# Optimization experiments

Hardware: AMD Instinct MI355X
Metric: run time of the kernel (lower is better)

## Reference

```python
import jax, jax.numpy as jnp
import numpy as np

B, C_MAX, T = 128, 272, 512
D1 = 320
NUM_SUBJECTS = 8
NUM_CHANNELS = [272, 256, 240, 224, 208, 270, 260, 248]


def setup_inputs() -> dict:
    key = jax.random.key(0)
    k_x, k_w, k_s = jax.random.split(key, 3)
    X = jax.random.normal(k_x, (B, C_MAX, T), dtype=jnp.float32)
    subject_idxs = jax.random.randint(k_s, (B,), 0, NUM_SUBJECTS)
    # Per-subject Conv1d(kernel=1, bias=False) weights, padded to C_MAX.
    # Original module only reads the first num_channels[s] input channels;
    # zeroing the padded columns reproduces that exactly.
    W = jax.random.normal(k_w, (NUM_SUBJECTS, D1, C_MAX), dtype=jnp.float32) * 0.02
    mask = np.zeros((NUM_SUBJECTS, 1, C_MAX), dtype=np.float32)
    for s, nc in enumerate(NUM_CHANNELS):
        mask[s, 0, :nc] = 1.0
    W = W * jnp.asarray(mask)
    return {"X": X, "subject_idxs": subject_idxs, "W": W}


def reference(X, subject_idxs, W):
    # Gather per-sample weight matrix [B, D1, C_MAX] by subject id, then
    # batched 1x1 conv == matmul over channels at every time step.
    Wsel = W[subject_idxs]                      # [B, D1, C]
    out = jnp.einsum("bdc,bct->bdt", Wsel, X)   # [B, D1, T]
    return out
```

## Files before the change

kernel.cpp:

```cpp
#include <hip/hip_runtime.h>

#define BB    128
#define CC    272
#define TT    512
#define DD1   320
#define KC    32
#define NCHUNK 9
#define NT    64
#define MT    160
#define LDA   40
#define LDB   40

typedef float  f32x4  __attribute__((ext_vector_type(4)));
typedef __bf16 bf16x4 __attribute__((ext_vector_type(4)));
typedef __bf16 bf16x8 __attribute__((ext_vector_type(8)));

#define BAR() asm volatile("s_waitcnt lgkmcnt(0)\ns_barrier" ::: "memory")

__global__ __launch_bounds__(256, 4)
void subj_conv_mfma(const float* __restrict__ X,
                    const int*   __restrict__ sidx,
                    const float* __restrict__ W,
                    float*       __restrict__ out) {
    const int b  = blockIdx.x;
    const int T0 = blockIdx.y * NT;
    const int d0 = blockIdx.z * MT;
    const int s  = sidx[b];

    __shared__ __bf16 As[MT * LDA];
    __shared__ __bf16 Bs[NT * LDB];

    const int tid  = threadIdx.x;
    const int lane = tid & 63;
    const int wv   = tid >> 6;
    const int wm   = wv & 1;
    const int wn   = wv >> 1;
    const int quad = lane >> 4;
    const int l16  = lane & 15;

    const float* Wb = W + ((size_t)s * DD1 + d0) * CC;
    const float* Xb = X + (size_t)b * CC * TT + T0;

    const int am  = tid >> 3;
    const int akk = (tid & 7) * 4;
    const int bcr = tid >> 4;
    const int bt  = (tid & 15) * 4;

    f32x4 acc[5][2];
#pragma unroll
    for (int mt = 0; mt < 5; ++mt) {
        acc[mt][0] = (f32x4){0.f, 0.f, 0.f, 0.f};
        acc[mt][1] = (f32x4){0.f, 0.f, 0.f, 0.f};
    }

    float4 pa[5];
    float4 pb[2];

    {
        const int c0 = 0;
#pragma unroll
        for (int p = 0; p < 5; ++p) {
            const int m = am + 32 * p;
            pa[p] = *(const float4*)(Wb + (size_t)m * CC + (c0 + akk));
        }
#pragma unroll
        for (int p = 0; p < 2; ++p) {
            const int c = c0 + bcr + 16 * p;
            pb[p] = *(const float4*)(Xb + (size_t)c * TT + bt);
        }
    }

    for (int kc = 0; kc < NCHUNK; ++kc) {
#pragma unroll
        for (int p = 0; p < 5; ++p) {
            const int m = am + 32 * p;
            bf16x4 h = {(__bf16)pa[p].x, (__bf16)pa[p].y,
                        (__bf16)pa[p].z, (__bf16)pa[p].w};
            *(bf16x4*)&As[m * LDA + akk] = h;
        }
#pragma unroll
        for (int p = 0; p < 2; ++p) {
            const int cr = bcr + 16 * p;
            Bs[(bt + 0) * LDB + cr] = (__bf16)pb[p].x;
            Bs[(bt + 1) * LDB + cr] = (__bf16)pb[p].y;
            Bs[(bt + 2) * LDB + cr] = (__bf16)pb[p].z;
            Bs[(bt + 3) * LDB + cr] = (__bf16)pb[p].w;
        }

        BAR();

        if (kc + 1 < NCHUNK) {
            const int c0 = (kc + 1) * KC;
#pragma unroll
            for (int p = 0; p < 5; ++p) {
                const int m = am + 32 * p;
                const int c = c0 + akk;
                float4 v = make_float4(0.f, 0.f, 0.f, 0.f);
                if (c < CC) v = *(const float4*)(Wb + (size_t)m * CC + c);
                pa[p] = v;
            }
#pragma unroll
            for (int p = 0; p < 2; ++p) {
                const int c = c0 + bcr + 16 * p;
                float4 v = make_float4(0.f, 0.f, 0.f, 0.f);
                if (c < CC) v = *(const float4*)(Xb + (size_t)c * TT + bt);
                pb[p] = v;
            }
        }

        bf16x8 bfr[2];
#pragma unroll
        for (int nt = 0; nt < 2; ++nt)
            bfr[nt] = *(const bf16x8*)&Bs[(wn * 32 + nt * 16 + l16) * LDB + quad * 8];

#pragma unroll
        for (int mt = 0; mt < 5; ++mt) {
            bf16x8 af = *(const bf16x8*)&As[(wm * 80 + mt * 16 + l16) * LDA + quad * 8];
#pragma unroll
            for (int nt = 0; nt < 2; ++nt)
                acc[mt][nt] = __builtin_amdgcn_mfma_f32_16x16x32_bf16(
                    af, bfr[nt], acc[mt][nt], 0, 0, 0);
        }

        BAR();
    }

#pragma unroll
    for (int mt = 0; mt < 5; ++mt) {
        const int d = d0 + wm * 80 + mt * 16 + quad * 4;
#pragma unroll
        for (int nt = 0; nt < 2; ++nt) {
            float* ob = out + ((size_t)b * DD1 + d) * TT + T0 + wn * 32 + nt * 16 + l16;
#pragma unroll
            for (int r = 0; r < 4; ++r)
                ob[(size_t)r * TT] = acc[mt][nt][r];
        }
    }
}

extern "C" void kernel_launch(void* const* d_in, const int* in_sizes, int n_in,
                              void* d_out, int out_size, void* d_ws, size_t ws_size,
                              hipStream_t stream) {
    const float* X    = (const float*)d_in[0];
    const int*   sidx = (const int*)  d_in[1];
    const float* W    = (const float*)d_in[2];
    float*       out  = (float*)d_out;

    dim3 grid(BB, TT / NT, 2);
    dim3 block(256);
    subj_conv_mfma<<<grid, block, 0, stream>>>(X, sidx, W, out);
}
```

Measured before the change: 168.2 us.

## Double-buffer LDS tiles and store X as fp32 row-major, converting on read

Adds two LDS buffers for both the W and X tiles so the next chunk is stored while the current one is consumed, cutting one barrier per iteration and looking two chunks ahead for global loads. The X tile is now kept in fp32 with its natural channel-major layout (padded stride 66) using vectorized float2 stores, instead of scattered transposed bf16 scalar stores. In exchange, each B fragment now takes eight scalar LDS reads plus conversions instead of one vector load, and LDS usage grows, which may reduce occupancy.

```diff
diff --git a/kernel.cpp b/kernel.cpp
--- a/kernel.cpp
+++ b/kernel.cpp
@@ -9,7 +9,7 @@
 #define NT    64
 #define MT    160
 #define LDA   40
-#define LDB   40
+#define LDB2  66
 
 typedef float  f32x4  __attribute__((ext_vector_type(4)));
 typedef __bf16 bf16x4 __attribute__((ext_vector_type(4)));
@@ -27,8 +27,8 @@
     const int d0 = blockIdx.z * MT;
     const int s  = sidx[b];
 
-    __shared__ __bf16 As[MT * LDA];
-    __shared__ __bf16 Bs[NT * LDB];
+    __shared__ __bf16 As[2][MT * LDA];
+    __shared__ float  Bs[2][KC * LDB2];
 
     const int tid  = threadIdx.x;
     const int lane = tid & 63;
@@ -56,73 +56,74 @@
     float4 pa[5];
     float4 pb[2];
 
-    {
-        const int c0 = 0;
+    auto load_chunk = [&](int c0) {
 #pragma unroll
         for (int p = 0; p < 5; ++p) {
             const int m = am + 32 * p;
-            pa[p] = *(const float4*)(Wb + (size_t)m * CC + (c0 + akk));
+            const int c = c0 + akk;
+            float4 v = make_float4(0.f, 0.f, 0.f, 0.f);
+            if (c < CC) v = *(const float4*)(Wb + (size_t)m * CC + c);
+            pa[p] = v;
         }
 #pragma unroll
         for (int p = 0; p < 2; ++p) {
             const int c = c0 + bcr + 16 * p;
-            pb[p] = *(const float4*)(Xb + (size_t)c * TT + bt);
+            float4 v = make_float4(0.f, 0.f, 0.f, 0.f);
+            if (c < CC) v = *(const float4*)(Xb + (size_t)c * TT + bt);
+            pb[p] = v;
         }
-    }
+    };
 
-    for (int kc = 0; kc < NCHUNK; ++kc) {
+    auto store_chunk = [&](int buf) {
 #pragma unroll
         for (int p = 0; p < 5; ++p) {
             const int m = am + 32 * p;
             bf16x4 h = {(__bf16)pa[p].x, (__bf16)pa[p].y,
                         (__bf16)pa[p].z, (__bf16)pa[p].w};
-            *(bf16x4*)&As[m * LDA + akk] = h;
+            *(bf16x4*)&As[buf][m * LDA + akk] = h;
         }
 #pragma unroll
         for (int p = 0; p < 2; ++p) {
             const int cr = bcr + 16 * p;
-            Bs[(bt + 0) * LDB + cr] = (__bf16)pb[p].x;
-            Bs[(bt + 1) * LDB + cr] = (__bf16)pb[p].y;
-            Bs[(bt + 2) * LDB + cr] = (__bf16)pb[p].z;
-            Bs[(bt + 3) * LDB + cr] = (__bf16)pb[p].w;
+            float* row = &Bs[buf][cr * LDB2 + bt];
+            *(float2*)(row + 0) = make_float2(pb[p].x, pb[p].y);
+            *(float2*)(row + 2) = make_float2(pb[p].z, pb[p].w);
         }
+    };
 
-        BAR();
+    load_chunk(0);
+    store_chunk(0);
+    load_chunk(KC);
+    BAR();
 
-        if (kc + 1 < NCHUNK) {
-            const int c0 = (kc + 1) * KC;
-#pragma unroll
-            for (int p = 0; p < 5; ++p) {
-                const int m = am + 32 * p;
-                const int c = c0 + akk;
-                float4 v = make_float4(0.f, 0.f, 0.f, 0.f);
-                if (c < CC) v = *(const float4*)(Wb + (size_t)m * CC + c);
-                pa[p] = v;
-            }
-#pragma unroll
-            for (int p = 0; p < 2; ++p) {
-                const int c = c0 + bcr + 16 * p;
-                float4 v = make_float4(0.f, 0.f, 0.f, 0.f);
-                if (c < CC) v = *(const float4*)(Xb + (size_t)c * TT + bt);
-                pb[p] = v;
-            }
-        }
+    for (int kc = 0; kc < NCHUNK; ++kc) {
+        const int cur = kc & 1;
 
         bf16x8 bfr[2];
 #pragma unroll
-        for (int nt = 0; nt < 2; ++nt)
-            bfr[nt] = *(const bf16x8*)&Bs[(wn * 32 + nt * 16 + l16) * LDB + quad * 8];
+        for (int nt = 0; nt < 2; ++nt) {
+            const int tcol = wn * 32 + nt * 16 + l16;
+            bf16x8 h;
+#pragma unroll
+            for (int j = 0; j < 8; ++j)
+                h[j] = (__bf16)Bs[cur][(quad * 8 + j) * LDB2 + tcol];
+            bfr[nt] = h;
+        }
 
 #pragma unroll
         for (int mt = 0; mt < 5; ++mt) {
-            bf16x8 af = *(const bf16x8*)&As[(wm * 80 + mt * 16 + l16) * LDA + quad * 8];
+            bf16x8 af = *(const bf16x8*)&As[cur][(wm * 80 + mt * 16 + l16) * LDA + quad * 8];
 #pragma unroll
             for (int nt = 0; nt < 2; ++nt)
                 acc[mt][nt] = __builtin_amdgcn_mfma_f32_16x16x32_bf16(
                     af, bfr[nt], acc[mt][nt], 0, 0, 0);
         }
 
-        BAR();
+        if (kc + 1 < NCHUNK) {
+            store_chunk(1 - cur);
+            if (kc + 2 < NCHUNK) load_chunk((kc + 2) * KC);
+            BAR();
+        }
     }
 
 #pragma unroll
```

After: 164.4 us. 2.2% less time.
